# Optimization experiments

Hardware: AMD Instinct MI355X
Metric: run time of the kernel (lower is better)

The kernel has to match this reference:

```python
import jax, jax.numpy as jnp
import numpy as np

NB_STEPS = 300  # quadrature steps hard-coded in EmbeddingNet.__init__
B, D, C = 2048, 128, 64  # batch, in_main(=in_embedding), out_embedding


def _glorot(key, shape):
    fan_in, fan_out = shape
    lim = (6.0 / (fan_in + fan_out)) ** 0.5
    return jax.random.uniform(key, shape, jnp.float32, -lim, lim)


def setup_inputs() -> dict:
    key = jax.random.key(0)
    ks = jax.random.split(key, 9)
    x = jax.random.uniform(ks[0], (B, D), jnp.float32)
    # embedding net: D -> 200 -> 200 -> C (ReLU after every layer)
    W1 = _glorot(ks[1], (D, 200)); b1 = jnp.zeros((200,), jnp.float32)
    W2 = _glorot(ks[2], (200, 200)); b2 = jnp.zeros((200,), jnp.float32)
    W3 = _glorot(ks[3], (200, C)); b3 = jnp.zeros((C,), jnp.float32)
    # UMNN integrand net: (D + C) -> 100 -> 100 -> 100 -> D, positive output via ELU+1
    U1 = _glorot(ks[4], (D + C, 100)); c1 = jnp.zeros((100,), jnp.float32)
    U2 = _glorot(ks[5], (100, 100)); c2 = jnp.zeros((100,), jnp.float32)
    U3 = _glorot(ks[6], (100, 100)); c3 = jnp.zeros((100,), jnp.float32)
    U4 = _glorot(ks[7], (100, D)); c4 = jnp.zeros((D,), jnp.float32)
    return {"x": x, "W1": W1, "b1": b1, "W2": W2, "b2": b2, "W3": W3, "b3": b3,
            "U1": U1, "c1": c1, "U2": U2, "c2": c2, "U3": U3, "c3": c3,
            "U4": U4, "c4": c4}


def _forward(x, W1, b1, W2, b2, W3, b3, U1, c1, U2, c2, U3, c3, U4, c4):
    # conditioning embedding h = embedding_net(x)
    h = jax.nn.relu(x @ W1 + b1)
    h = jax.nn.relu(h @ W2 + b2)
    h = jax.nn.relu(h @ W3 + b3)                                   # (B, C)
    # UMNN: F(x,h) = int_0^1 f(t*x, h) . x dt, f > 0 via ELU+1 => monotone in each x_d.
    # All NB_STEPS quadrature points evaluated as one batched GEMM (the 'fast' form
    # of the original Python-level 300-step loop). Midpoint rule on (0,1).
    t = (jnp.arange(NB_STEPS, dtype=x.dtype) + 0.5) / NB_STEPS     # (T,)
    X = t[None, :, None] * x[:, None, :]                           # (B, T, D) points on path 0 -> x
    Hc = jnp.broadcast_to(h[:, None, :], (x.shape[0], NB_STEPS, h.shape[1]))
    z = jnp.concatenate([X, Hc], axis=-1)                          # (B, T, D+C)
    a = jax.nn.relu(z @ U1 + c1)
    a = jax.nn.relu(a @ U2 + c2)
    a = jax.nn.relu(a @ U3 + c3)
    f = jax.nn.elu(a @ U4 + c4) + 1.0                              # (B, T, D), strictly positive
    F = jnp.einsum('btd,bd->b', f, x) / NB_STEPS                   # line-integral quadrature
    return jax.nn.sigmoid(F)[:, None]                              # (B, 1)


def reference(x, W1, b1, W2, b2, W3, b3, U1, c1, U2, c2, U3, c3, U4, c4):
    return _forward(x, W1, b1, W2, b2, W3, b3, U1, c1, U2, c2, U3, c3, U4, c4)
```

## Files before the change

kernel.cpp:

```cpp
#include <hip/hip_runtime.h>

typedef __attribute__((ext_vector_type(8))) short bf16x8;
typedef __attribute__((ext_vector_type(4))) float f32x4;
typedef __attribute__((ext_vector_type(16))) float f32x16;
typedef int v2i __attribute__((ext_vector_type(2)));

union U4B { unsigned u[4]; bf16x8 v; };

__device__ __forceinline__ unsigned short f2bf(float f) {
    union { float f; unsigned u; } v; v.f = f;
    unsigned r = v.u + 0x7fffu + ((v.u >> 16) & 1u);
    return (unsigned short)(r >> 16);
}
__device__ __forceinline__ float bf2f(unsigned short s) {
    union { unsigned u; float f; } v; v.u = ((unsigned)s) << 16; return v.f;
}
__device__ __forceinline__ unsigned pkbf(float a, float b) {
    unsigned r;
    asm("v_cvt_pk_bf16_f32 %0, %1, %2" : "=v"(r) : "v"(a), "v"(b));
    return r;
}
__device__ __forceinline__ bf16x8 packhalf(const f32x16& a, int base) {
    unsigned u  = pkbf(a[base + 0], a[base + 1]);
    unsigned u2 = pkbf(a[base + 2], a[base + 3]);
    unsigned v  = pkbf(a[base + 4], a[base + 5]);
    unsigned v2 = pkbf(a[base + 6], a[base + 7]);
    v2i r1 = __builtin_amdgcn_permlane32_swap(u, v, false, false);
    v2i r2 = __builtin_amdgcn_permlane32_swap(u2, v2, false, false);
    U4B b; b.u[0] = r1.x; b.u[1] = r2.x; b.u[2] = r1.y; b.u[3] = r2.y;
    return b.v;
}
__device__ __forceinline__ f32x16 zero16() {
    f32x16 v;
#pragma unroll
    for (int i = 0; i < 16; ++i) v[i] = 0.f;
    return v;
}

#define BATCH   2048
#define TSTEPS  300
#define ROWS_PB 8
#define WM_OFF   0
#define G_OFF    98304
#define E_OFF    622592
#define EW1_OFF  1146880
#define EU1X_OFF 1204224
#define EW2_OFF  1236992
#define EW3_OFF  1351680
#define EU1H_OFF 1384448
#define EB_OFF   1417216
#define OFF_X   98304
#define OFF_G   102400
#define OFF_E   106496
#define OFF_P   110592
#define SMEM_M  110656
#define EACT    114688
#define EB1     131072
#define EB2     131968
#define EB3     132864
#define EC1     133120
#define SMEM_E  133632

__global__ __launch_bounds__(256) void prep_kernel(
    const float* __restrict__ W1, const float* __restrict__ b1,
    const float* __restrict__ W2, const float* __restrict__ b2,
    const float* __restrict__ W3, const float* __restrict__ b3,
    const float* __restrict__ U1, const float* __restrict__ c1,
    const float* __restrict__ U2, const float* __restrict__ c2,
    const float* __restrict__ U3, const float* __restrict__ c3,
    const float* __restrict__ U4, const float* __restrict__ c4,
    unsigned char* __restrict__ ws)
{
    const int NT = 128 * 256;
    const int gid = blockIdx.x * 256 + threadIdx.x;
    unsigned short* w16 = (unsigned short*)ws;

    for (int j = gid; j < 3 * 128 * 128; j += NT) {
        int m = j >> 14, r = j & 16383;
        int k = r >> 7, n = r & 127;
        float v = 0.f;
        if (m == 2) {
            if (k < 100)       v = U4[k * 128 + n];
            else if (k == 100) v = c4[n];
        } else {
            const float* U = m ? U3 : U2;
            const float* c = m ? c3 : c2;
            if (k < 100)       { if (n < 100) v = U[k * 100 + n]; }
            else if (k == 100) { if (n < 100) v = c[n]; else if (n == 100) v = 1.f; }
        }
        w16[(WM_OFF >> 1) + m * 16384 + n * 128 + k] = f2bf(v);
    }
    for (int j = gid; j < 128 * 224; j += NT) {
        int k = j / 224, n = j % 224;
        float v = (n < 200) ? W1[k * 200 + n] : 0.f;
        w16[(EW1_OFF >> 1) + n * 128 + k] = f2bf(v);
    }
    for (int j = gid; j < 128 * 128; j += NT) {
        int k = j >> 7, n = j & 127;
        float v = (n < 100) ? U1[k * 100 + n] : 0.f;
        w16[(EU1X_OFF >> 1) + n * 128 + k] = f2bf(v);
    }
    for (int j = gid; j < 128 * 128; j += NT) {
        int k = j >> 7, n = j & 127;
        float v = (k < 64 && n < 100) ? U1[(128 + k) * 100 + n] : 0.f;
        w16[(EU1H_OFF >> 1) + n * 128 + k] = f2bf(v);
    }
    for (int j = gid; j < 256 * 224; j += NT) {
        int k = j / 224, n = j % 224;
        float v = (k < 200 && n < 200) ? W2[k * 200 + n] : 0.f;
        w16[(EW2_OFF >> 1) + n * 256 + k] = f2bf(v);
    }
    for (int j = gid; j < 256 * 64; j += NT) {
        int k = j >> 6, n = j & 63;
        float v = (k < 200) ? W3[k * 64 + n] : 0.f;
        w16[(EW3_OFF >> 1) + n * 256 + k] = f2bf(v);
    }
    if (gid < 640) {
        int j = gid; float v;
        if (j < 224)      v = (j < 200) ? b1[j] : 0.f;
        else if (j < 448) v = (j - 224 < 200) ? b2[j - 224] : 0.f;
        else if (j < 512) v = b3[j - 448];
        else              v = (j - 512 < 100) ? c1[j - 512] : 0.f;
        ((float*)(ws + EB_OFF))[j] = v;
    }
}

__device__ __forceinline__ void act_store(char* act, int l31, int f, int hi,
                                          const f32x16& a) {
#pragma unroll
    for (int r = 0; r < 16; r += 2) {
        int n = 32 * f + (r & 3) + 8 * (r >> 2) + 4 * hi;
        unsigned u = pkbf(fmaxf(a[r], 0.f), fmaxf(a[r + 1], 0.f));
        *(unsigned*)(act + l31 * 512 + ((n * 2) ^ ((l31 & 7) << 4))) = u;
    }
}
__device__ __forceinline__ bf16x8 act_read(const char* act, int l31, int ks, int hi) {
    return *(const bf16x8*)(act + l31 * 512 + ((ks * 32 + hi * 16) ^ ((l31 & 7) << 4)));
}

__global__ __launch_bounds__(256) void embed2(
    const float* __restrict__ x, unsigned char* __restrict__ ws)
{
    __shared__ __align__(16) char sm[SMEM_E];
    char* act = sm + EACT;
    const int tid = threadIdx.x;
    const int lane = tid & 63, wid = tid >> 6;
    const int l31 = lane & 31, hi = lane >> 5;
    const int brow = blockIdx.x * 32 + l31;
    const int sw8 = (l31 & 15) << 4;
    const int sw9 = (l31 & 31) << 4;

    for (int i = tid; i < 640; i += 256)
        ((float*)(sm + EB1))[i] = ((const float*)(ws + EB_OFF))[i];

    {
        const uint4* s1 = (const uint4*)(ws + EW1_OFF);
        for (int ci = tid; ci < 3584; ci += 256) {
            int n = ci >> 4, part = ci & 15;
            *(uint4*)(sm + n * 256 + ((part * 16) ^ ((n & 15) << 4))) = s1[ci];
        }
        const uint4* s2 = (const uint4*)(ws + EU1X_OFF);
        for (int ci = tid; ci < 2048; ci += 256) {
            int n = ci >> 4, part = ci & 15;
            *(uint4*)(sm + 57344 + n * 256 + ((part * 16) ^ ((n & 15) << 4))) = s2[ci];
        }
    }

    bf16x8 Bx[8];
    {
        const float* xr = x + brow * 128;
#pragma unroll
        for (int ks = 0; ks < 8; ++ks) {
            const int k0 = ks * 16 + hi * 8;
            f32x4 a = *(const f32x4*)(xr + k0);
            f32x4 b = *(const f32x4*)(xr + k0 + 4);
            U4B u;
            u.u[0] = pkbf(a[0], a[1]); u.u[1] = pkbf(a[2], a[3]);
            u.u[2] = pkbf(b[0], b[1]); u.u[3] = pkbf(b[2], b[3]);
            Bx[ks] = u.v;
        }
    }
    __syncthreads();

    unsigned short* g16 = (unsigned short*)(ws + G_OFF);
    unsigned short* e16 = (unsigned short*)(ws + E_OFF);

    {
        f32x16 ag = zero16();
#pragma unroll
        for (int ks = 0; ks < 8; ++ks) {
            bf16x8 a = *(const bf16x8*)(sm + 57344 + (32 * wid + l31) * 256 + ((ks * 32 + hi * 16) ^ sw8));
            ag = __builtin_amdgcn_mfma_f32_32x32x16_bf16(a, Bx[ks], ag, 0, 0, 0);
        }
#pragma unroll
        for (int r = 0; r < 16; r += 2) {
            int n = 32 * wid + (r & 3) + 8 * (r >> 2) + 4 * hi;
            *(unsigned*)(g16 + brow * 128 + n) = pkbf(ag[r], ag[r + 1]);
        }
    }

    for (int f = wid; f < 7; f += 4) {
        f32x16 acc;
#pragma unroll
        for (int r = 0; r < 16; ++r)
            acc[r] = ((float*)(sm + EB1))[32 * f + (r & 3) + 8 * (r >> 2) + 4 * hi];
#pragma unroll
        for (int ks = 0; ks < 8; ++ks) {
            bf16x8 a = *(const bf16x8*)(sm + (32 * f + l31) * 256 + ((ks * 32 + hi * 16) ^ sw8));
            acc = __builtin_amdgcn_mfma_f32_32x32x16_bf16(a, Bx[ks], acc, 0, 0, 0);
        }
        act_store(act, l31, f, hi, acc);
    }
    __syncthreads();

    bf16x8 Bh[13];
#pragma unroll
    for (int ks = 0; ks < 13; ++ks) Bh[ks] = act_read(act, l31, ks, hi);
    __syncthreads();
    {
        const uint4* s3 = (const uint4*)(ws + EW2_OFF);
        for (int ci = tid; ci < 7168; ci += 256) {
            int n = ci >> 5, part = ci & 31;
            *(uint4*)(sm + n * 512 + ((part * 16) ^ ((n & 31) << 4))) = s3[ci];
        }
    }
    __syncthreads();

    for (int f = wid; f < 7; f += 4) {
        f32x16 acc;
#pragma unroll
        for (int r = 0; r < 16; ++r)
            acc[r] = ((float*)(sm + EB2))[32 * f + (r & 3) + 8 * (r >> 2) + 4 * hi];
#pragma unroll
        for (int ks = 0; ks < 13; ++ks) {
            bf16x8 a = *(const bf16x8*)(sm + (32 * f + l31) * 512 + ((ks * 32 + hi * 16) ^ sw9));
            acc = __builtin_amdgcn_mfma_f32_32x32x16_bf16(a, Bh[ks], acc, 0, 0, 0);
        }
        act_store(act, l31, f, hi, acc);
    }
    __syncthreads();

    bf16x8 Bh2[13];
#pragma unroll
    for (int ks = 0; ks < 13; ++ks) Bh2[ks] = act_read(act, l31, ks, hi);
    __syncthreads();
    {
        const uint4* s4 = (const uint4*)(ws + EW3_OFF);
        for (int ci = tid; ci < 2048; ci += 256) {
            int n = ci >> 5, part = ci & 31;
            *(uint4*)(sm + n * 512 + ((part * 16) ^ ((n & 31) << 4))) = s4[ci];
        }
        const uint4* s5 = (const uint4*)(ws + EU1H_OFF);
        for (int ci = tid; ci < 2048; ci += 256) {
            int n = ci >> 4, part = ci & 15;
            *(uint4*)(sm + 32768 + n * 256 + ((part * 16) ^ ((n & 15) << 4))) = s5[ci];
        }
    }
    __syncthreads();

    for (int f = wid; f < 2; f += 4) {
        f32x16 acc;
#pragma unroll
        for (int r = 0; r < 16; ++r)
            acc[r] = ((float*)(sm + EB3))[32 * f + (r & 3) + 8 * (r >> 2) + 4 * hi];
#pragma unroll
        for (int ks = 0; ks < 13; ++ks) {
            bf16x8 a = *(const bf16x8*)(sm + (32 * f + l31) * 512 + ((ks * 32 + hi * 16) ^ sw9));
            acc = __builtin_amdgcn_mfma_f32_32x32x16_bf16(a, Bh2[ks], acc, 0, 0, 0);
        }
        act_store(act, l31, f, hi, acc);
    }
    __syncthreads();

    {
        f32x16 ae;
#pragma unroll
        for (int r = 0; r < 16; ++r)
            ae[r] = ((float*)(sm + EC1))[32 * wid + (r & 3) + 8 * (r >> 2) + 4 * hi];
        bf16x8 B4[4];
#pragma unroll
        for (int ks = 0; ks < 4; ++ks) B4[ks] = act_read(act, l31, ks, hi);
#pragma unroll
        for (int ks = 0; ks < 4; ++ks) {
            bf16x8 a = *(const bf16x8*)(sm + 32768 + (32 * wid + l31) * 256 + ((ks * 32 + hi * 16) ^ sw8));
            ae = __builtin_amdgcn_mfma_f32_32x32x16_bf16(a, B4[ks], ae, 0, 0, 0);
        }
#pragma unroll
        for (int r = 0; r < 16; r += 2) {
            int n = 32 * wid + (r & 3) + 8 * (r >> 2) + 4 * hi;
            float v0 = ae[r], v1 = ae[r + 1];
            if (wid == 3 && hi == 1 && r == 0) v0 = 1.f;
            *(unsigned*)(e16 + brow * 128 + n) = pkbf(v0, v1);
        }
    }
}

__global__ __launch_bounds__(1024)
__attribute__((amdgpu_waves_per_eu(4, 4))) void umnn_main(
    const float* __restrict__ x,
    const unsigned char* __restrict__ ws, float* __restrict__ out)
{
    __shared__ __align__(16) char sm[SMEM_M];
    float* sX = (float*)(sm + OFF_X);
    float* sG = (float*)(sm + OFF_G);
    float* sE = (float*)(sm + OFF_E);
    float* sP = (float*)(sm + OFF_P);
    const int tid = threadIdx.x;
    const int lane = tid & 63, wid = tid >> 6;
    const int l31 = lane & 31, hi = lane >> 5;
    const int b8 = blockIdx.x * ROWS_PB;

    {
        const uint4* src = (const uint4*)(ws + WM_OFF);
        for (int ci = tid; ci < 6144; ci += 1024) {
            int m = ci >> 11, wi = ci & 2047, n = wi >> 4, part = wi & 15;
            uint4 v = src[ci];
            *(uint4*)(sm + m * 32768 + n * 256 + ((part * 16) ^ ((n & 15) << 4))) = v;
        }
        const unsigned short* g16 = (const unsigned short*)(ws + G_OFF);
        const unsigned short* e16 = (const unsigned short*)(ws + E_OFF);
        {
            int r = tid >> 7, d = tid & 127;
            sX[tid] = x[(b8 + r) * 128 + d];
            sG[tid] = bf2f(g16[(b8 + r) * 128 + d]);
            sE[tid] = bf2f(e16[(b8 + r) * 128 + d]);
        }
    }
    __syncthreads();

    const int row = wid >> 1, half = wid & 1;
    const float* gR = sG + row * 128;
    const float* eR = sE + row * 128;
    const float* xR = sX + row * 128;
    const int sw = (l31 & 15) << 4;
    const char* wB2 = sm;
    const char* wB3 = sm + 32768;
    const char* wB4 = sm + 65536;

    float sumF = 0.f;

#pragma unroll 1
    for (int s = 0; s < 5; ++s) {
        const int t = half * 160 + s * 32 + l31;
        const float tt = ((float)t + 0.5f) * (1.f / 300.f);

        bf16x8 B[7];
#pragma unroll
        for (int ks = 0; ks < 7; ++ks) {
            const int k0 = ks * 16 + hi * 8;
            f32x4 g0 = *(const f32x4*)(gR + k0);
            f32x4 g1 = *(const f32x4*)(gR + k0 + 4);
            f32x4 e0 = *(const f32x4*)(eR + k0);
            f32x4 e1 = *(const f32x4*)(eR + k0 + 4);
            float a0 = fmaxf(fmaf(tt, g0[0], e0[0]), 0.f);
            float a1 = fmaxf(fmaf(tt, g0[1], e0[1]), 0.f);
            float a2 = fmaxf(fmaf(tt, g0[2], e0[2]), 0.f);
            float a3 = fmaxf(fmaf(tt, g0[3], e0[3]), 0.f);
            float a4 = fmaxf(fmaf(tt, g1[0], e1[0]), 0.f);
            float a5 = fmaxf(fmaf(tt, g1[1], e1[1]), 0.f);
            float a6 = fmaxf(fmaf(tt, g1[2], e1[2]), 0.f);
            float a7 = fmaxf(fmaf(tt, g1[3], e1[3]), 0.f);
            U4B u;
            u.u[0] = pkbf(a0, a1); u.u[1] = pkbf(a2, a3);
            u.u[2] = pkbf(a4, a5); u.u[3] = pkbf(a6, a7);
            B[ks] = u.v;
        }

#pragma unroll
        for (int L = 0; L < 2; ++L) {
            const char* wb = (L == 0) ? wB2 : wB3;
            f32x16 acc[4];
#pragma unroll
            for (int f = 0; f < 4; ++f) acc[f] = zero16();
#pragma unroll
            for (int ks = 0; ks < 7; ++ks) {
                const int ko = ks * 32 + hi * 16;
#pragma unroll
                for (int f = 0; f < 4; ++f) {
                    bf16x8 a = *(const bf16x8*)(wb + (32 * f + l31) * 256 + (ko ^ sw));
                    acc[f] = __builtin_amdgcn_mfma_f32_32x32x16_bf16(a, B[ks], acc[f], 0, 0, 0);
                }
            }
#pragma unroll
            for (int f = 0; f < 4; ++f) {
#pragma unroll
                for (int r = 0; r < 16; ++r) acc[f][r] = fmaxf(acc[f][r], 0.f);
                B[2 * f] = packhalf(acc[f], 0);
                if (f < 3) B[2 * f + 1] = packhalf(acc[f], 8);
            }
        }

        float sdot = 0.f;
#pragma unroll
        for (int f = 0; f < 4; ++f) {
            f32x16 acc = zero16();
#pragma unroll
            for (int ks = 0; ks < 7; ++ks) {
                const int ko = ks * 32 + hi * 16;
                bf16x8 a = *(const bf16x8*)(wB4 + (32 * f + l31) * 256 + (ko ^ sw));
                acc = __builtin_amdgcn_mfma_f32_32x32x16_bf16(a, B[ks], acc, 0, 0, 0);
            }
#pragma unroll
            for (int q = 0; q < 4; ++q) {
                const int n0 = f * 32 + q * 8 + hi * 4;
                f32x4 xv = *(const f32x4*)(xR + n0);
#pragma unroll
                for (int i = 0; i < 4; ++i) {
                    float p = acc[q * 4 + i];
                    float fv = (p > 0.f) ? (p + 1.f) : __expf(p);
                    sdot = fmaf(fv, xv[i], sdot);
                }
            }
        }
        if (t < TSTEPS) sumF += sdot;
    }

#pragma unroll
    for (int off = 32; off >= 1; off >>= 1) sumF += __shfl_xor(sumF, off);
    if (lane == 0) sP[wid] = sumF;
    __syncthreads();
    if (tid < ROWS_PB) {
        float F = (sP[tid * 2] + sP[tid * 2 + 1]) * (1.f / 300.f);
        out[b8 + tid] = 1.f / (1.f + __expf(-F));
    }
}

extern "C" void kernel_launch(void* const* d_in, const int* in_sizes, int n_in,
                              void* d_out, int out_size, void* d_ws, size_t ws_size,
                              hipStream_t stream)
{
    const float* x  = (const float*)d_in[0];
    const float* W1 = (const float*)d_in[1];
    const float* b1 = (const float*)d_in[2];
    const float* W2 = (const float*)d_in[3];
    const float* b2 = (const float*)d_in[4];
    const float* W3 = (const float*)d_in[5];
    const float* b3 = (const float*)d_in[6];
    const float* U1 = (const float*)d_in[7];
    const float* c1 = (const float*)d_in[8];
    const float* U2 = (const float*)d_in[9];
    const float* c2 = (const float*)d_in[10];
    const float* U3 = (const float*)d_in[11];
    const float* c3 = (const float*)d_in[12];
    const float* U4 = (const float*)d_in[13];
    const float* c4 = (const float*)d_in[14];
    float* out = (float*)d_out;
    unsigned char* ws = (unsigned char*)d_ws;

    prep_kernel<<<128, 256, 0, stream>>>(W1, b1, W2, b2, W3, b3, U1, c1,
                                         U2, c2, U3, c3, U4, c4, ws);
    embed2<<<64, 256, 0, stream>>>(x, ws);
    umnn_main<<<BATCH / ROWS_PB, 1024, 0, stream>>>(x, ws, out);
}
```

Before: 160.9 us.

## Fuse weight prep into embedding kernel, converting weights directly into LDS

Merges the separate weight-preparation kernel with the embedding kernel. 64 blocks now read fp32 embedding weights straight from global memory, convert them to bf16 and write them into swizzled LDS, and 8 extra blocks convert the UMNN main-net weights into the workspace. This removes one kernel launch and the workspace round trip for the embedding weights. In exchange, every embedding block now redundantly converts all embedding weights with scalar 2-byte LDS stores and strided global reads.

```diff
diff --git a/kernel.cpp b/kernel.cpp
--- a/kernel.cpp
+++ b/kernel.cpp
@@ -43,12 +43,6 @@
 #define WM_OFF   0
 #define G_OFF    98304
 #define E_OFF    622592
-#define EW1_OFF  1146880
-#define EU1X_OFF 1204224
-#define EW2_OFF  1236992
-#define EW3_OFF  1351680
-#define EU1H_OFF 1384448
-#define EB_OFF   1417216
 #define OFF_X   98304
 #define OFF_G   102400
 #define OFF_E   106496
@@ -61,7 +55,21 @@
 #define EC1     133120
 #define SMEM_E  133632
 
-__global__ __launch_bounds__(256) void prep_kernel(
+__device__ __forceinline__ void act_store(char* act, int l31, int f, int hi,
+                                          const f32x16& a) {
+#pragma unroll
+    for (int r = 0; r < 16; r += 2) {
+        int n = 32 * f + (r & 3) + 8 * (r >> 2) + 4 * hi;
+        unsigned u = pkbf(fmaxf(a[r], 0.f), fmaxf(a[r + 1], 0.f));
+        *(unsigned*)(act + l31 * 512 + ((n * 2) ^ ((l31 & 7) << 4))) = u;
+    }
+}
+__device__ __forceinline__ bf16x8 act_read(const char* act, int l31, int ks, int hi) {
+    return *(const bf16x8*)(act + l31 * 512 + ((ks * 32 + hi * 16) ^ ((l31 & 7) << 4)));
+}
+
+__global__ __launch_bounds__(256) void fused_pre(
+    const float* __restrict__ x,
     const float* __restrict__ W1, const float* __restrict__ b1,
     const float* __restrict__ W2, const float* __restrict__ b2,
     const float* __restrict__ W3, const float* __restrict__ b3,
@@ -71,99 +79,52 @@
     const float* __restrict__ U4, const float* __restrict__ c4,
     unsigned char* __restrict__ ws)
 {
-    const int NT = 128 * 256;
-    const int gid = blockIdx.x * 256 + threadIdx.x;
-    unsigned short* w16 = (unsigned short*)ws;
-
-    for (int j = gid; j < 3 * 128 * 128; j += NT) {
-        int m = j >> 14, r = j & 16383;
-        int k = r >> 7, n = r & 127;
-        float v = 0.f;
-        if (m == 2) {
-            if (k < 100)       v = U4[k * 128 + n];
-            else if (k == 100) v = c4[n];
-        } else {
-            const float* U = m ? U3 : U2;
-            const float* c = m ? c3 : c2;
-            if (k < 100)       { if (n < 100) v = U[k * 100 + n]; }
-            else if (k == 100) { if (n < 100) v = c[n]; else if (n == 100) v = 1.f; }
-        }
-        w16[(WM_OFF >> 1) + m * 16384 + n * 128 + k] = f2bf(v);
-    }
-    for (int j = gid; j < 128 * 224; j += NT) {
-        int k = j / 224, n = j % 224;
-        float v = (n < 200) ? W1[k * 200 + n] : 0.f;
-        w16[(EW1_OFF >> 1) + n * 128 + k] = f2bf(v);
-    }
-    for (int j = gid; j < 128 * 128; j += NT) {
-        int k = j >> 7, n = j & 127;
-        float v = (n < 100) ? U1[k * 100 + n] : 0.f;
-        w16[(EU1X_OFF >> 1) + n * 128 + k] = f2bf(v);
-    }
-    for (int j = gid; j < 128 * 128; j += NT) {
-        int k = j >> 7, n = j & 127;
-        float v = (k < 64 && n < 100) ? U1[(128 + k) * 100 + n] : 0.f;
-        w16[(EU1H_OFF >> 1) + n * 128 + k] = f2bf(v);
-    }
-    for (int j = gid; j < 256 * 224; j += NT) {
-        int k = j / 224, n = j % 224;
-        float v = (k < 200 && n < 200) ? W2[k * 200 + n] : 0.f;
-        w16[(EW2_OFF >> 1) + n * 256 + k] = f2bf(v);
-    }
-    for (int j = gid; j < 256 * 64; j += NT) {
-        int k = j >> 6, n = j & 63;
-        float v = (k < 200) ? W3[k * 64 + n] : 0.f;
-        w16[(EW3_OFF >> 1) + n * 256 + k] = f2bf(v);
-    }
-    if (gid < 640) {
-        int j = gid; float v;
-        if (j < 224)      v = (j < 200) ? b1[j] : 0.f;
-        else if (j < 448) v = (j - 224 < 200) ? b2[j - 224] : 0.f;
-        else if (j < 512) v = b3[j - 448];
-        else              v = (j - 512 < 100) ? c1[j - 512] : 0.f;
-        ((float*)(ws + EB_OFF))[j] = v;
-    }
-}
-
-__device__ __forceinline__ void act_store(char* act, int l31, int f, int hi,
-                                          const f32x16& a) {
-#pragma unroll
-    for (int r = 0; r < 16; r += 2) {
-        int n = 32 * f + (r & 3) + 8 * (r >> 2) + 4 * hi;
-        unsigned u = pkbf(fmaxf(a[r], 0.f), fmaxf(a[r + 1], 0.f));
-        *(unsigned*)(act + l31 * 512 + ((n * 2) ^ ((l31 & 7) << 4))) = u;
-    }
-}
-__device__ __forceinline__ bf16x8 act_read(const char* act, int l31, int ks, int hi) {
-    return *(const bf16x8*)(act + l31 * 512 + ((ks * 32 + hi * 16) ^ ((l31 & 7) << 4)));
-}
-
-__global__ __launch_bounds__(256) void embed2(
-    const float* __restrict__ x, unsigned char* __restrict__ ws)
-{
     __shared__ __align__(16) char sm[SMEM_E];
+    const int tid = threadIdx.x;
+
+    if (blockIdx.x >= 64) {
+        const int part = blockIdx.x - 64;
+        unsigned short* w16 = (unsigned short*)ws;
+        for (int j = part * 6144 + tid; j < (part + 1) * 6144; j += 256) {
+            int m = j >> 14, r = j & 16383;
+            int k = r >> 7, n = r & 127;
+            float v = 0.f;
+            if (m == 2) {
+                if (k < 100)       v = U4[k * 128 + n];
+                else if (k == 100) v = c4[n];
+            } else {
+                const float* U = m ? U3 : U2;
+                const float* c = m ? c3 : c2;
+                if (k < 100)       { if (n < 100) v = U[k * 100 + n]; }
+                else if (k == 100) { if (n < 100) v = c[n]; else if (n == 100) v = 1.f; }
+            }
+            w16[(WM_OFF >> 1) + m * 16384 + n * 128 + k] = f2bf(v);
+        }
+        return;
+    }
+
     char* act = sm + EACT;
-    const int tid = threadIdx.x;
     const int lane = tid & 63, wid = tid >> 6;
     const int l31 = lane & 31, hi = lane >> 5;
     const int brow = blockIdx.x * 32 + l31;
     const int sw8 = (l31 & 15) << 4;
     const int sw9 = (l31 & 31) << 4;
 
-    for (int i = tid; i < 640; i += 256)
-        ((float*)(sm + EB1))[i] = ((const float*)(ws + EB_OFF))[i];
-
-    {
-        const uint4* s1 = (const uint4*)(ws + EW1_OFF);
-        for (int ci = tid; ci < 3584; ci += 256) {
-            int n = ci >> 4, part = ci & 15;
-            *(uint4*)(sm + n * 256 + ((part * 16) ^ ((n & 15) << 4))) = s1[ci];
-        }
-        const uint4* s2 = (const uint4*)(ws + EU1X_OFF);
-        for (int ci = tid; ci < 2048; ci += 256) {
-            int n = ci >> 4, part = ci & 15;
-            *(uint4*)(sm + 57344 + n * 256 + ((part * 16) ^ ((n & 15) << 4))) = s2[ci];
-        }
+    if (tid < 224) ((float*)(sm + EB1))[tid] = (tid < 200) ? b1[tid] : 0.f;
+    if (tid < 224) ((float*)(sm + EB2))[tid] = (tid < 200) ? b2[tid] : 0.f;
+    if (tid < 64)  ((float*)(sm + EB3))[tid] = b3[tid];
+    if (tid < 128) ((float*)(sm + EC1))[tid] = (tid < 100) ? c1[tid] : 0.f;
+
+    for (int k = 0; k < 128; ++k) {
+        if (tid < 224) {
+            float v = (tid < 200) ? W1[k * 200 + tid] : 0.f;
+            *(unsigned short*)(sm + tid * 256 + ((k * 2) ^ ((tid & 15) << 4))) = f2bf(v);
+        }
+    }
+    for (int kk = 0; kk < 64; ++kk) {
+        int k = kk * 2 + (tid >> 7), n = tid & 127;
+        float v = (n < 100) ? U1[k * 100 + n] : 0.f;
+        *(unsigned short*)(sm + 57344 + n * 256 + ((k * 2) ^ ((n & 15) << 4))) = f2bf(v);
     }
 
     bf16x8 Bx[8];
@@ -217,11 +178,10 @@
 #pragma unroll
     for (int ks = 0; ks < 13; ++ks) Bh[ks] = act_read(act, l31, ks, hi);
     __syncthreads();
-    {
-        const uint4* s3 = (const uint4*)(ws + EW2_OFF);
-        for (int ci = tid; ci < 7168; ci += 256) {
-            int n = ci >> 5, part = ci & 31;
-            *(uint4*)(sm + n * 512 + ((part * 16) ^ ((n & 31) << 4))) = s3[ci];
+    for (int k = 0; k < 256; ++k) {
+        if (tid < 224) {
+            float v = (k < 200 && tid < 200) ? W2[k * 200 + tid] : 0.f;
+            *(unsigned short*)(sm + tid * 512 + ((k * 2) ^ ((tid & 31) << 4))) = f2bf(v);
         }
     }
     __syncthreads();
@@ -244,17 +204,15 @@
 #pragma unroll
     for (int ks = 0; ks < 13; ++ks) Bh2[ks] = act_read(act, l31, ks, hi);
     __syncthreads();
-    {
-        const uint4* s4 = (const uint4*)(ws + EW3_OFF);
-        for (int ci = tid; ci < 2048; ci += 256) {
-            int n = ci >> 5, part = ci & 31;
-            *(uint4*)(sm + n * 512 + ((part * 16) ^ ((n & 31) << 4))) = s4[ci];
-        }
-        const uint4* s5 = (const uint4*)(ws + EU1H_OFF);
-        for (int ci = tid; ci < 2048; ci += 256) {
-            int n = ci >> 4, part = ci & 15;
-            *(uint4*)(sm + 32768 + n * 256 + ((part * 16) ^ ((n & 15) << 4))) = s5[ci];
-        }
+    for (int kk = 0; kk < 64; ++kk) {
+        int k = kk * 4 + (tid >> 6), n = tid & 63;
+        float v = (k < 200) ? W3[k * 64 + n] : 0.f;
+        *(unsigned short*)(sm + n * 512 + ((k * 2) ^ ((n & 31) << 4))) = f2bf(v);
+    }
+    for (int kk = 0; kk < 64; ++kk) {
+        int k = kk * 2 + (tid >> 7), n = tid & 127;
+        float v = (k < 64 && n < 100) ? U1[(128 + k) * 100 + n] : 0.f;
+        *(unsigned short*)(sm + 32768 + n * 256 + ((k * 2) ^ ((n & 15) << 4))) = f2bf(v);
     }
     __syncthreads();
 
@@ -447,8 +405,7 @@
     float* out = (float*)d_out;
     unsigned char* ws = (unsigned char*)d_ws;
 
-    prep_kernel<<<128, 256, 0, stream>>>(W1, b1, W2, b2, W3, b3, U1, c1,
-                                         U2, c2, U3, c3, U4, c4, ws);
-    embed2<<<64, 256, 0, stream>>>(x, ws);
+    fused_pre<<<72, 256, 0, stream>>>(x, W1, b1, W2, b2, W3, b3, U1, c1,
+                                      U2, c2, U3, c3, U4, c4, ws);
     umnn_main<<<BATCH / ROWS_PB, 1024, 0, stream>>>(x, ws, out);
 }
```

Result: slower. 263.4 us (+63.6%).
